# Performance work log

Hardware: AMD Instinct MI355X
Metric: run time of the kernel (lower is better)

## Reference

```python
import jax, jax.numpy as jnp
import numpy as np
from jax import lax

DN = ('NCHW', 'OIHW', 'NCHW')

def conv2d(x, w, b=None, padding='SAME'):
    y = lax.conv_general_dilated(x, w, (1, 1), padding, dimension_numbers=DN)
    if b is not None:
        y = y + b[None, :, None, None]
    return y

def setup_inputs() -> dict:
    key = jax.random.key(0)
    ks = jax.random.split(key, 9)
    B, C, H, W = 8, 256, 64, 64
    s = lambda fan: 1.0 / np.sqrt(fan)
    return {
        'x': jax.random.normal(ks[0], (B, C, H, W), jnp.float32),
        'qkv_w': jax.random.normal(ks[1], (3 * C, C, 1, 1), jnp.float32) * s(C),
        'qkv_b': jnp.zeros((3 * C,), jnp.float32),
        'out_w': jax.random.normal(ks[2], (C, C, 1, 1), jnp.float32) * s(C),
        'out_b': jnp.zeros((C,), jnp.float32),
        'd1_w': jax.random.normal(ks[3], (8, 1, 3, 3), jnp.float32) * s(9),
        'd1_b': jnp.zeros((8,), jnp.float32),
        'd2_w': jax.random.normal(ks[4], (1, 8, 3, 3), jnp.float32) * s(72),
        'd2_b': jnp.zeros((1,), jnp.float32),
    }

def reference(x, qkv_w, qkv_b, out_w, out_b, d1_w, d1_b, d2_w, d2_b):
    B, C, H, W = x.shape
    N = H * W
    # gradient-energy (Laplacian) density proxy
    gray = x.mean(axis=1, keepdims=True)                      # [B,1,H,W]
    lap_k = jnp.array([[0., -1., 0.], [-1., 4., -1.], [0., -1., 0.]],
                      dtype=x.dtype).reshape(1, 1, 3, 3)
    lap = conv2d(gray, lap_k)                                 # [B,1,H,W]
    h = jax.nn.relu(conv2d(jnp.abs(lap), d1_w, d1_b))         # [B,8,H,W]
    density = jax.nn.sigmoid(conv2d(h, d2_w, d2_b))           # [B,1,H,W]
    # qkv via 1x1 conv == channel matmul
    qkv = jnp.einsum('oc,bchw->bohw', qkv_w[:, :, 0, 0], x) + qkv_b[None, :, None, None]
    q, k, v = jnp.split(qkv, 3, axis=1)                       # each [B,C,H,W]
    q = q.reshape(B, C, N).transpose(0, 2, 1)                 # [B,N,C]
    k = k.reshape(B, C, N)                                    # [B,C,N]
    v = v.reshape(B, C, N).transpose(0, 2, 1)                 # [B,N,C]
    attn = jnp.einsum('bnc,bcm->bnm', q, k) * (float(C) ** -0.5)  # [B,Nq,Nk]
    temperature = 1.0 + 2.0 * (1.0 - density.reshape(B, 1, N))    # per-key [B,1,Nk]
    attn = jax.nn.softmax(attn / temperature, axis=-1)
    out = jnp.einsum('bnm,bmc->bnc', attn, v)                 # [B,N,C]
    out = out.transpose(0, 2, 1).reshape(B, C, H, W)
    out = jnp.einsum('oc,bchw->bohw', out_w[:, :, 0, 0], out) + out_b[None, :, None, None]
    return out + x
```

## Files before the change

kernel.cpp:

```cpp
#include <hip/hip_runtime.h>
#include <hip/hip_bf16.h>

typedef __attribute__((ext_vector_type(8))) short s16x8;
typedef __attribute__((ext_vector_type(4))) float f32x4;
typedef __attribute__((ext_vector_type(16))) float f32x16;
typedef __attribute__((ext_vector_type(4))) unsigned short us4;
typedef __attribute__((ext_vector_type(4))) unsigned int u32x4;

#define MFMA16(a,b,c) __builtin_amdgcn_mfma_f32_16x16x32_bf16((a),(b),(c),0,0,0)
#define MFMA32(a,b,c) __builtin_amdgcn_mfma_f32_32x32x16_bf16((a),(b),(c),0,0,0)

__device__ __forceinline__ float b2f(unsigned short u){
  union{unsigned u; float f;} v; v.u = ((unsigned)u)<<16; return v.f;
}
__device__ __forceinline__ unsigned short f2b(float f){
  union{float f; unsigned u;} v; v.f = f;
  unsigned r = v.u + 0x7fffu + ((v.u>>16)&1u);
  return (unsigned short)(r>>16);
}
__device__ __forceinline__ unsigned cvt_pk_bf16(float lo, float hi){
  unsigned r;
  asm volatile("v_cvt_pk_bf16_f32 %0, %1, %2" : "=v"(r) : "v"(lo), "v"(hi));
  return r;
}

__device__ __forceinline__ void gl_lds16(const void* gp, void* lp){
  __builtin_amdgcn_global_load_lds((const __attribute__((address_space(1))) void*)gp,
                                   (__attribute__((address_space(3))) void*)lp, 16, 0, 0);
}

__device__ __forceinline__ void stage_64x256(void* lds, const unsigned short* g, int stride){
  const int t = threadIdx.x, wv = t>>6;
  #pragma unroll
  for (int i=0;i<8;++i){
    int ch = i*256 + t;
    int row = ch>>5, cc = ch&31, sc = cc ^ (row&7);
    gl_lds16((const char*)(g + (size_t)row*stride) + sc*16,
             (char*)lds + (((size_t)i*256 + wv*64)<<4));
  }
}
__device__ __forceinline__ void stage16KB(void* lds, const unsigned short* g){
  const int tid = threadIdx.x;
  #pragma unroll
  for (int i=0;i<2;++i){
    int ch = i*512 + tid;
    gl_lds16((const char*)(g + (size_t)ch*8), (char*)lds + (size_t)ch*16);
  }
}

__global__ void k_cvt(const float* __restrict__ src, unsigned short* __restrict__ dst){
  int i = blockIdx.x*256 + threadIdx.x;
  f32x4 v = *(const f32x4*)(src + (size_t)i*4);
  us4 o;
  #pragma unroll
  for (int r=0;r<4;++r) o[r] = f2b(v[r]);
  *(us4*)(dst + (size_t)i*4) = o;
}

__global__ void k_transpose(const float* __restrict__ xg, unsigned short* __restrict__ Xtg,
                            float* __restrict__ gray4){
  __shared__ unsigned short T[64*68];
  __shared__ float psum[4*64];
  const int nb = blockIdx.x, cb = blockIdx.y, b = blockIdx.z;
  const int n0 = nb*64, c0 = cb*64;
  const int t = threadIdx.x;
  #pragma unroll
  for (int i=0;i<4;++i){
    int idx = i*256 + t;
    int c = idx>>4, k4 = idx&15;
    f32x4 v = *(const f32x4*)(xg + ((size_t)(b*256 + c0 + c))*4096 + n0 + k4*4);
    us4 o;
    #pragma unroll
    for (int r=0;r<4;++r) o[r] = f2b(v[r]);
    *(us4*)&T[c*68 + k4*4] = o;
  }
  __syncthreads();
  #pragma unroll
  for (int i=0;i<2;++i){
    int idx = i*256 + t;
    int n = idx>>3, ck = idx&7;
    unsigned short vv[8];
    #pragma unroll
    for (int j=0;j<8;++j) vv[j] = T[(ck*8+j)*68 + n];
    *(u32x4*)(Xtg + ((size_t)(b*4096 + n0 + n))*256 + c0 + ck*8) = *(const u32x4*)vv;
  }
  {
    int j = t&63, q = t>>6;
    float s = 0.f;
    #pragma unroll
    for (int c16=0;c16<16;++c16) s += b2f(T[(q*16+c16)*68 + j]);
    psum[q*64 + j] = s;
  }
  __syncthreads();
  if (t < 64){
    float s = psum[t] + psum[64+t] + psum[128+t] + psum[192+t];
    gray4[((size_t)(cb*8 + b))*4096 + n0 + t] = s;
  }
}

__global__ __launch_bounds__(256) void k_density(const float* __restrict__ gray4,
    const float* __restrict__ w1, const float* __restrict__ b1,
    const float* __restrict__ w2, const float* __restrict__ b2_,
    float* __restrict__ sc2){
  __shared__ float gf[4096];
  __shared__ float la[4096];
  __shared__ unsigned short hb[8*4096];
  const int b = blockIdx.x, t = threadIdx.x;
  #pragma unroll
  for (int i=0;i<16;++i){
    int px = i*256 + t;
    float s = gray4[(size_t)(0*8+b)*4096 + px] + gray4[(size_t)(1*8+b)*4096 + px]
            + gray4[(size_t)(2*8+b)*4096 + px] + gray4[(size_t)(3*8+b)*4096 + px];
    gf[px] = s * (1.f/256.f);
  }
  __syncthreads();
  #pragma unroll
  for (int i=0;i<16;++i){
    int px = i*256 + t;
    int hh = px>>6, ww = px&63;
    float c = gf[px];
    float up = hh>0  ? gf[px-64] : 0.f;
    float dn = hh<63 ? gf[px+64] : 0.f;
    float lf = ww>0  ? gf[px-1]  : 0.f;
    float rt = ww<63 ? gf[px+1]  : 0.f;
    la[px] = fabsf(4.f*c - up - dn - lf - rt);
  }
  __syncthreads();
  float w1r[72], b1r[8];
  #pragma unroll
  for (int k=0;k<72;++k) w1r[k] = w1[k];
  #pragma unroll
  for (int j=0;j<8;++j) b1r[j] = b1[j];
  #pragma unroll
  for (int i=0;i<16;++i){
    int px = i*256 + t;
    int hh = px>>6, ww = px&63;
    float tap[9];
    #pragma unroll
    for (int dy=-1;dy<=1;++dy)
      #pragma unroll
      for (int dx=-1;dx<=1;++dx){
        int y=hh+dy, x2=ww+dx;
        tap[(dy+1)*3+dx+1] = (y>=0&&y<64&&x2>=0&&x2<64)? la[y*64+x2] : 0.f;
      }
    #pragma unroll
    for (int j=0;j<8;++j){
      float a = b1r[j];
      #pragma unroll
      for (int k=0;k<9;++k) a += w1r[j*9+k]*tap[k];
      hb[j*4096 + px] = f2b(fmaxf(a, 0.f));
    }
  }
  __syncthreads();
  float w2r[72], b20 = b2_[0];
  #pragma unroll
  for (int k=0;k<72;++k) w2r[k] = w2[k];
  #pragma unroll
  for (int i=0;i<16;++i){
    int px = i*256 + t;
    int hh = px>>6, ww = px&63;
    float a = b20;
    #pragma unroll
    for (int j=0;j<8;++j){
      #pragma unroll
      for (int dy=-1;dy<=1;++dy)
        #pragma unroll
        for (int dx=-1;dx<=1;++dx){
          int y=hh+dy, x2=ww+dx;
          if (y>=0&&y<64&&x2>=0&&x2<64) a += w2r[j*9+(dy+1)*3+(dx+1)]*b2f(hb[j*4096 + y*64+x2]);
        }
    }
    float sig = 1.f/(1.f+__expf(-a));
    sc2[(size_t)b*4096 + px] = 0.09016844f/(3.f - 2.f*sig);
  }
}

__global__ __launch_bounds__(256,2) void k_gemm_qkv(const unsigned short* __restrict__ Wg,
    const unsigned short* __restrict__ Xtg, const float* __restrict__ biasg,
    unsigned short* __restrict__ Qo, unsigned short* __restrict__ Ko, unsigned short* __restrict__ Vto){
  __shared__ unsigned short Xl[64*256];
  __shared__ unsigned short Wl[64*256];
  const int nt_ = blockIdx.x, b = blockIdx.y;
  const int n0 = nt_*64;
  stage_64x256(Xl, Xtg + ((size_t)(b*4096 + n0))*256, 256);
  const int t = threadIdx.x, w = t>>6, lane = t&63, lam = lane&15, lg = lane>>4;
  f32x4 zz = {0.f,0.f,0.f,0.f};
  for (int at=0; at<12; ++at){
    const int a0 = at*64;
    stage_64x256(Wl, Wg + (size_t)a0*256, 256);
    __syncthreads();
    f32x4 acc[4] = {zz,zz,zz,zz};
    #pragma unroll
    for (int u=0;u<8;++u){
      int ar = 16*w + lam;
      s16x8 af = *(const s16x8*)((const char*)Wl + ar*512 + ((64*u+16*lg) ^ ((ar&7)<<4)));
      #pragma unroll
      for (int ct=0;ct<4;++ct){
        int br = 16*ct + lam;
        s16x8 bf = *(const s16x8*)((const char*)Xl + br*512 + ((64*u+16*lg) ^ ((br&7)<<4)));
        acc[ct] = MFMA16(af, bf, acc[ct]);
      }
    }
    const int ob = a0 + 16*w + 4*lg;
    f32x4 bias4 = *(const f32x4*)(biasg + ob);
    #pragma unroll
    for (int ct=0;ct<4;++ct){
      int n = n0 + 16*ct + lam;
      us4 ov;
      #pragma unroll
      for (int r=0;r<4;++r) ov[r] = f2b(acc[ct][r] + bias4[r]);
      if (a0 < 256){
        *(us4*)(Qo + ((size_t)(b*4096 + n))*256 + ob) = ov;
      } else if (a0 < 512){
        int c4 = ob - 256;
        size_t idx = (((size_t)(b*128 + (n>>5))*1024) + (c4>>3)*32 + (n&31))*8 + (c4&7);
        *(us4*)(Ko + idx) = ov;
      } else {
        int c0v = ob - 512;
        size_t base = ((size_t)(b*128 + (n>>5))*1024 + ((n&31)>>3)*256)*8 + (n&7);
        #pragma unroll
        for (int r=0;r<4;++r)
          Vto[base + (size_t)(c0v+r)*8] = ov[r];
      }
    }
    __syncthreads();
  }
}

__global__ __launch_bounds__(512,2) void k_attn(const unsigned short* __restrict__ Qg,
    const unsigned short* __restrict__ Kg, const unsigned short* __restrict__ Vtg,
    const float* __restrict__ Sg, unsigned short* __restrict__ AOt){
  __shared__ __align__(16) char SL[132096];
  unsigned short* Kl = (unsigned short*)SL;
  unsigned short* Vl = (unsigned short*)(SL + 65536);
  float* mlb = (float*)(SL + 131072);
  float* Ob  = (float*)SL;

  const int tid = threadIdx.x, w = tid>>6, lane = tid&63, l31 = lane&31, h = lane>>5;
  const int g = w>>2;
  const int bid = blockIdx.x;
  const int b = bid&7, qt = bid>>3;
  const int qbase = qt*128 + (w&3)*32;

  const unsigned short* KgB = Kg  + (size_t)b*128*8192;
  const unsigned short* VtB = Vtg + (size_t)b*128*8192;
  const float* SgB = Sg + (size_t)b*4096 + g*2048;

  s16x8 qf[16];
  {
    const unsigned short* qp = Qg + ((size_t)(b*4096 + qbase + l31))*256 + 8*h;
    #pragma unroll
    for (int u=0;u<16;++u) qf[u] = *(const s16x8*)(qp + 16*u);
  }
  f32x16 oa[8];
  #pragma unroll
  for (int nb=0;nb<8;++nb)
    #pragma unroll
    for (int i=0;i<16;++i) oa[nb][i]=0.f;
  float m_run = 0.f, l_run = 0.f;

  #define KBUF(bu,gr) (Kl + ((bu)*2+(gr))*8192)
  #define VBUF(bu,gr) (Vl + ((bu)*2+(gr))*8192)

  stage16KB(KBUF(0,0), KgB);
  stage16KB(KBUF(0,1), KgB + (size_t)64*8192);
  stage16KB(VBUF(0,0), VtB);
  stage16KB(VBUF(0,1), VtB + (size_t)64*8192);
  __syncthreads();

  int cur = 0;
  for (int t=0; t<64; ++t){
    if (t < 63){
      stage16KB(KBUF(cur^1,0), KgB + (size_t)(t+1)*8192);
      stage16KB(KBUF(cur^1,1), KgB + (size_t)(64+t+1)*8192);
      stage16KB(VBUF(cur^1,0), VtB + (size_t)(t+1)*8192);
      stage16KB(VBUF(cur^1,1), VtB + (size_t)(64+t+1)*8192);
    }
    const char* Kc = (const char*)KBUF(cur,g);
    const char* Vc = (const char*)VBUF(cur,g);

    f32x4 sv[4];
    {
      const float* Sp = SgB + t*32;
      #pragma unroll
      for (int j=0;j<4;++j) sv[j] = *(const f32x4*)(Sp + 8*j + 4*h);
    }

    f32x16 st;
    #pragma unroll
    for (int i=0;i<16;++i) st[i]=0.f;
    __builtin_amdgcn_s_setprio(1);
    #pragma unroll
    for (int u=0;u<16;++u){
      s16x8 kf = *(const s16x8*)(Kc + (((2*u+h)*32 + l31)<<4));
      st = MFMA32(kf, qf[u], st);
    }
    __builtin_amdgcn_s_setprio(0);

    float pm[16];
    #pragma unroll
    for (int j=0;j<4;++j)
      #pragma unroll
      for (int i=0;i<4;++i) pm[4*j+i] = st[4*j+i]*sv[j][i];

    float mx[8];
    #pragma unroll
    for (int i=0;i<8;++i) mx[i] = fmaxf(pm[i], pm[8+i]);
    #pragma unroll
    for (int i=0;i<4;++i) mx[i] = fmaxf(mx[i], mx[4+i]);
    float tmax = fmaxf(fmaxf(mx[0],mx[1]), fmaxf(mx[2],mx[3]));
    if (__any(tmax > m_run + 11.5415603f)){
      tmax = fmaxf(tmax, __shfl_xor(tmax, 32));
      float mnew = fmaxf(m_run, tmax);
      float fs = exp2f(m_run - mnew);
      m_run = mnew;
      l_run *= fs;
      float fr[16];
      #pragma unroll
      for (int r=0;r<16;++r) fr[r] = __shfl(fs, (r&3)+8*(r>>2)+4*h);
      #pragma unroll
      for (int nb=0;nb<8;++nb)
        #pragma unroll
        for (int r=0;r<16;++r) oa[nb][r] *= fr[r];
    }
    float pe[16];
    #pragma unroll
    for (int i=0;i<16;++i) pe[i] = exp2f(pm[i] - m_run);
    {
      float sm[8];
      #pragma unroll
      for (int i=0;i<8;++i) sm[i] = pe[i] + pe[8+i];
      #pragma unroll
      for (int i=0;i<4;++i) sm[i] += sm[4+i];
      float rs = (sm[0]+sm[1])+(sm[2]+sm[3]);
      rs += __shfl_xor(rs, 32);
      l_run += rs;
    }

    unsigned pq[8];
    #pragma unroll
    for (int j=0;j<4;++j){
      pq[2*j]   = cvt_pk_bf16(pe[4*j],   pe[4*j+1]);
      pq[2*j+1] = cvt_pk_bf16(pe[4*j+2], pe[4*j+3]);
    }

    __builtin_amdgcn_s_setprio(1);
    #pragma unroll
    for (int ks=0;ks<2;++ks){
      const int j0 = 2*ks, j1 = 2*ks+1;
      unsigned s0 = h ? pq[2*j0]   : pq[2*j1];
      unsigned s1 = h ? pq[2*j0+1] : pq[2*j1+1];
      unsigned r0 = (unsigned)__shfl_xor((int)s0, 32);
      unsigned r1 = (unsigned)__shfl_xor((int)s1, 32);
      union { unsigned u[4]; s16x8 v; } pa;
      pa.u[0] = h ? r0 : pq[2*j0];
      pa.u[1] = h ? r1 : pq[2*j0+1];
      pa.u[2] = h ? pq[2*j1]   : r0;
      pa.u[3] = h ? pq[2*j1+1] : r1;
      #pragma unroll
      for (int nb=0;nb<8;++nb){
        s16x8 vf = *(const s16x8*)(Vc + (((2*ks+h)*256 + 32*nb + l31)<<4));
        oa[nb] = MFMA32(pa.v, vf, oa[nb]);
      }
    }
    __builtin_amdgcn_s_setprio(0);

    __syncthreads();
    cur ^= 1;
  }

  if (g == 1){
    if (h == 0){
      mlb[((w-4)*32 + l31)*2]   = m_run;
      mlb[((w-4)*32 + l31)*2+1] = l_run;
    }
    float* Ow = Ob + (size_t)(w-4)*32*256;
    #pragma unroll
    for (int nb=0;nb<8;++nb)
      #pragma unroll
      for (int r=0;r<16;++r){
        int qr = (r&3)+8*(r>>2)+4*h;
        Ow[qr*256 + 32*nb + l31] = oa[nb][r];
      }
  }
  __syncthreads();
  if (g == 0){
    const float* Or = Ob + (size_t)w*32*256;
    #pragma unroll
    for (int r=0;r<16;++r){
      int qr = (r&3)+8*(r>>2)+4*h;
      float m0r = __shfl(m_run, qr);
      float l0r = __shfl(l_run, qr);
      float m1r = mlb[(w*32+qr)*2];
      float l1r = mlb[(w*32+qr)*2+1];
      float M = fmaxf(m0r, m1r);
      float a0 = exp2f(m0r - M), a1 = exp2f(m1r - M);
      float inv = 1.f/(l0r*a0 + l1r*a1);
      a0 *= inv; a1 *= inv;
      unsigned short* dst = AOt + ((size_t)(b*4096 + qbase + qr))*256 + l31;
      #pragma unroll
      for (int nb=0;nb<8;++nb){
        float v = oa[nb][r]*a0 + Or[qr*256 + 32*nb + l31]*a1;
        dst[32*nb] = f2b(v);
      }
    }
  }
  #undef KBUF
  #undef VBUF
}

__global__ __launch_bounds__(256,2) void k_gemm_out(const unsigned short* __restrict__ Ag,
    const unsigned short* __restrict__ Bg, const float* __restrict__ biasg,
    const float* __restrict__ xg, float* __restrict__ outg){
  __shared__ unsigned short Al[64*256];
  __shared__ unsigned short Bl[64*256];
  const int at = blockIdx.x, b = blockIdx.y;
  const int a0 = at*64;
  stage_64x256(Al, Ag + ((size_t)(b*4096 + a0))*256, 256);
  const int t = threadIdx.x, w = t>>6, lane = t&63, lam = lane&15, lg = lane>>4;
  f32x4 zz = {0.f,0.f,0.f,0.f};
  for (int bt=0; bt<4; ++bt){
    const int o0 = bt*64;
    stage_64x256(Bl, Bg + (size_t)o0*256, 256);
    __syncthreads();
    f32x4 acc[4] = {zz,zz,zz,zz};
    #pragma unroll
    for (int u=0;u<8;++u){
      int ar = 16*w + lam;
      s16x8 af = *(const s16x8*)((const char*)Al + ar*512 + ((64*u+16*lg) ^ ((ar&7)<<4)));
      #pragma unroll
      for (int ct=0;ct<4;++ct){
        int br = 16*ct + lam;
        s16x8 bf = *(const s16x8*)((const char*)Bl + br*512 + ((64*u+16*lg) ^ ((br&7)<<4)));
        acc[ct] = MFMA16(af, bf, acc[ct]);
      }
    }
    #pragma unroll
    for (int ct=0;ct<4;++ct){
      int o = o0 + 16*ct + lam;
      float ob_ = biasg[o];
      size_t base = ((size_t)(b*256 + o))*4096 + a0 + 16*w + 4*lg;
      f32x4 xv = *(const f32x4*)(xg + base);
      f32x4 ov;
      #pragma unroll
      for (int r=0;r<4;++r) ov[r] = acc[ct][r] + ob_ + xv[r];
      *(f32x4*)(outg + base) = ov;
    }
    __syncthreads();
  }
}

extern "C" void kernel_launch(void* const* d_in, const int* in_sizes, int n_in,
                              void* d_out, int out_size, void* d_ws, size_t ws_size,
                              hipStream_t stream){
  const float* x     = (const float*)d_in[0];
  const float* qkv_w = (const float*)d_in[1];
  const float* qkv_b = (const float*)d_in[2];
  const float* out_w = (const float*)d_in[3];
  const float* out_b = (const float*)d_in[4];
  const float* d1_w  = (const float*)d_in[5];
  const float* d1_b  = (const float*)d_in[6];
  const float* d2_w  = (const float*)d_in[7];
  const float* d2_b  = (const float*)d_in[8];
  float* out = (float*)d_out;

  char* p = (char*)d_ws;
  const size_t BIG = (size_t)8*4096*256*2;
  unsigned short* Xt = (unsigned short*)p; p += BIG;
  unsigned short* Q  = (unsigned short*)p; p += BIG;
  unsigned short* K  = (unsigned short*)p; p += BIG;
  unsigned short* Vt = (unsigned short*)p; p += BIG;
  unsigned short* Wq = (unsigned short*)p; p += (size_t)768*256*2;
  unsigned short* Wo = (unsigned short*)p; p += (size_t)256*256*2;
  float* gray4 = (float*)p; p += (size_t)4*8*4096*4;
  float* sc    = (float*)p; p += (size_t)8*4096*4;

  k_cvt      <<<dim3(192),    256, 0, stream>>>(qkv_w, Wq);
  k_cvt      <<<dim3(64),     256, 0, stream>>>(out_w, Wo);
  k_transpose<<<dim3(64,4,8), 256, 0, stream>>>(x, Xt, gray4);
  k_density  <<<dim3(8),      256, 0, stream>>>(gray4, d1_w, d1_b, d2_w, d2_b, sc);
  k_gemm_qkv <<<dim3(64,8),   256, 0, stream>>>(Wq, Xt, qkv_b, Q, K, Vt);
  k_attn     <<<dim3(256),    512, 0, stream>>>(Q, K, Vt, sc, Xt);
  k_gemm_out <<<dim3(64,8),   256, 0, stream>>>(Xt, Wo, out_b, x, out);
}
```

Measured before the change: 278.1 us.

## Fuse output projection GEMM into attention kernel epilogue

The attention kernel now keeps the normalized 128x256 output tile in LDS in a bf16 MFMA-friendly layout and multiplies it by the out-projection weights (staged into LDS in two halves) with 32x32 MFMAs. It then adds bias and the residual and writes the final output directly. This removes the separate k_gemm_out launch and the round trip of the attention output through global memory. The costs are extra LDS staging and syncs at the end of each attention block, and output stores that are scalar and strided across channels.

After: 288.8 us. 3.8% more time.

```diff
diff --git a/kernel.cpp b/kernel.cpp
--- a/kernel.cpp
+++ b/kernel.cpp
@@ -55,6 +55,18 @@
   #pragma unroll
   for (int r=0;r<4;++r) o[r] = f2b(v[r]);
   *(us4*)(dst + (size_t)i*4) = o;
+}
+
+__global__ void k_cvt_wo(const float* __restrict__ src, unsigned short* __restrict__ dst){
+  int j = blockIdx.x*256 + threadIdx.x;
+  int flat = j*4;
+  int o = flat>>8, c = flat&255;
+  f32x4 v = *(const f32x4*)(src + flat);
+  us4 p;
+  #pragma unroll
+  for (int r=0;r<4;++r) p[r] = f2b(v[r]);
+  size_t idx = (size_t)(o>>5)*8192 + (size_t)(c>>3)*256 + (o&31)*8 + (c&7);
+  *(us4*)(dst + idx) = p;
 }
 
 __global__ void k_transpose(const float* __restrict__ xg, unsigned short* __restrict__ Xtg,
@@ -229,12 +241,16 @@
 
 __global__ __launch_bounds__(512,2) void k_attn(const unsigned short* __restrict__ Qg,
     const unsigned short* __restrict__ Kg, const unsigned short* __restrict__ Vtg,
-    const float* __restrict__ Sg, unsigned short* __restrict__ AOt){
+    const float* __restrict__ Sg, const unsigned short* __restrict__ WoG,
+    const float* __restrict__ obias, const float* __restrict__ xg,
+    float* __restrict__ outg){
   __shared__ __align__(16) char SL[132096];
   unsigned short* Kl = (unsigned short*)SL;
   unsigned short* Vl = (unsigned short*)(SL + 65536);
   float* mlb = (float*)(SL + 131072);
   float* Ob  = (float*)SL;
+  unsigned short* AOl = (unsigned short*)SL;
+  unsigned short* WoL = (unsigned short*)(SL + 65536);
 
   const int tid = threadIdx.x, w = tid>>6, lane = tid&63, l31 = lane&31, h = lane>>5;
   const int g = w>>2;
@@ -397,57 +413,70 @@
       float a0 = exp2f(m0r - M), a1 = exp2f(m1r - M);
       float inv = 1.f/(l0r*a0 + l1r*a1);
       a0 *= inv; a1 *= inv;
-      unsigned short* dst = AOt + ((size_t)(b*4096 + qbase + qr))*256 + l31;
-      #pragma unroll
-      for (int nb=0;nb<8;++nb){
-        float v = oa[nb][r]*a0 + Or[qr*256 + 32*nb + l31]*a1;
-        dst[32*nb] = f2b(v);
+      #pragma unroll
+      for (int nb=0;nb<8;++nb)
+        oa[nb][r] = oa[nb][r]*a0 + Or[qr*256 + 32*nb + l31]*a1;
+    }
+  }
+  __syncthreads();
+
+  if (g == 0){
+    #pragma unroll
+    for (int nb=0;nb<8;++nb){
+      #pragma unroll
+      for (int r=0;r<16;++r){
+        int qr = (r&3)+8*(r>>2)+4*h;
+        int c = 32*nb + l31;
+        AOl[(size_t)w*8192 + ((c>>3)*32 + qr)*8 + (c&7)] = f2b(oa[nb][r]);
+      }
+    }
+  } else {
+    int tl = tid - 256;
+    #pragma unroll
+    for (int i=0;i<16;++i){
+      int ch = i*256 + tl;
+      gl_lds16((const char*)(WoG + (size_t)ch*8), (char*)WoL + (size_t)ch*16);
+    }
+  }
+  __syncthreads();
+
+  #pragma unroll
+  for (int half=0; half<2; ++half){
+    if (half){
+      __syncthreads();
+      #pragma unroll
+      for (int i=0;i<8;++i){
+        int ch = i*512 + tid;
+        gl_lds16((const char*)(WoG + (size_t)32768 + (size_t)ch*8), (char*)WoL + (size_t)ch*16);
+      }
+      __syncthreads();
+    }
+    #pragma unroll
+    for (int rep=0; rep<2; ++rep){
+      int tile = w*2 + rep;
+      int nt2 = tile & 3, ot = tile >> 2;
+      f32x16 acc;
+      #pragma unroll
+      for (int i=0;i<16;++i) acc[i] = 0.f;
+      __builtin_amdgcn_s_setprio(1);
+      #pragma unroll
+      for (int u=0;u<16;++u){
+        s16x8 af = *(const s16x8*)((const char*)WoL + ot*16384 + (((2*u+h)*32 + l31)<<4));
+        s16x8 bf = *(const s16x8*)((const char*)AOl + nt2*16384 + (((2*u+h)*32 + l31)<<4));
+        acc = MFMA32(af, bf, acc);
+      }
+      __builtin_amdgcn_s_setprio(0);
+      #pragma unroll
+      for (int r=0;r<16;++r){
+        int o_g = half*128 + ot*32 + (r&3)+8*(r>>2)+4*h;
+        int n_g = qt*128 + nt2*32 + l31;
+        size_t base = ((size_t)(b*256 + o_g))*4096 + n_g;
+        outg[base] = acc[r] + obias[o_g] + xg[base];
       }
     }
   }
   #undef KBUF
   #undef VBUF
-}
-
-__global__ __launch_bounds__(256,2) void k_gemm_out(const unsigned short* __restrict__ Ag,
-    const unsigned short* __restrict__ Bg, const float* __restrict__ biasg,
-    const float* __restrict__ xg, float* __restrict__ outg){
-  __shared__ unsigned short Al[64*256];
-  __shared__ unsigned short Bl[64*256];
-  const int at = blockIdx.x, b = blockIdx.y;
-  const int a0 = at*64;
-  stage_64x256(Al, Ag + ((size_t)(b*4096 + a0))*256, 256);
-  const int t = threadIdx.x, w = t>>6, lane = t&63, lam = lane&15, lg = lane>>4;
-  f32x4 zz = {0.f,0.f,0.f,0.f};
-  for (int bt=0; bt<4; ++bt){
-    const int o0 = bt*64;
-    stage_64x256(Bl, Bg + (size_t)o0*256, 256);
-    __syncthreads();
-    f32x4 acc[4] = {zz,zz,zz,zz};
-    #pragma unroll
-    for (int u=0;u<8;++u){
-      int ar = 16*w + lam;
-      s16x8 af = *(const s16x8*)((const char*)Al + ar*512 + ((64*u+16*lg) ^ ((ar&7)<<4)));
-      #pragma unroll
-      for (int ct=0;ct<4;++ct){
-        int br = 16*ct + lam;
-        s16x8 bf = *(const s16x8*)((const char*)Bl + br*512 + ((64*u+16*lg) ^ ((br&7)<<4)));
-        acc[ct] = MFMA16(af, bf, acc[ct]);
-      }
-    }
-    #pragma unroll
-    for (int ct=0;ct<4;++ct){
-      int o = o0 + 16*ct + lam;
-      float ob_ = biasg[o];
-      size_t base = ((size_t)(b*256 + o))*4096 + a0 + 16*w + 4*lg;
-      f32x4 xv = *(const f32x4*)(xg + base);
-      f32x4 ov;
-      #pragma unroll
-      for (int r=0;r<4;++r) ov[r] = acc[ct][r] + ob_ + xv[r];
-      *(f32x4*)(outg + base) = ov;
-    }
-    __syncthreads();
-  }
 }
 
 extern "C" void kernel_launch(void* const* d_in, const int* in_sizes, int n_in,
@@ -476,10 +505,9 @@
   float* sc    = (float*)p; p += (size_t)8*4096*4;
 
   k_cvt      <<<dim3(192),    256, 0, stream>>>(qkv_w, Wq);
-  k_cvt      <<<dim3(64),     256, 0, stream>>>(out_w, Wo);
+  k_cvt_wo   <<<dim3(64),     256, 0, stream>>>(out_w, Wo);
   k_transpose<<<dim3(64,4,8), 256, 0, stream>>>(x, Xt, gray4);
   k_density  <<<dim3(8),      256, 0, stream>>>(gray4, d1_w, d1_b, d2_w, d2_b, sc);
   k_gemm_qkv <<<dim3(64,8),   256, 0, stream>>>(Wq, Xt, qkv_b, Q, K, Vt);
-  k_attn     <<<dim3(256),    512, 0, stream>>>(Q, K, Vt, sc, Xt);
-  k_gemm_out <<<dim3(64,8),   256, 0, stream>>>(Xt, Wo, out_b, x, out);
-}
+  k_attn     <<<dim3(256),    512, 0, stream>>>(Q, K, Vt, sc, Wo, out_b, x, out);
+}
```
